# Performance work log

Hardware: AMD Instinct MI355X
Metric: run time of the kernel (lower is better)

## Reference

```python
import jax, jax.numpy as jnp
import numpy as np

B, T, D, K = 4, 2048, 1024, 64


def _spectral_filters(seq_len, k):
    # Hankel matrix Z_ij = 2 / ((i+j)^3 - (i+j)), top-k eig-pairs scaled by sigma^0.25
    e = np.arange(1, seq_len + 1, dtype=np.float64)
    ipj = e[:, None] + e[None, :]
    Z = 2.0 / (ipj ** 3 - ipj)
    sig, phi = np.linalg.eigh(Z)
    sig_k = np.clip(sig[-k:], 1e-9, None)
    return (phi[:, -k:] * sig_k ** 0.25).astype(np.float32)


def setup_inputs() -> dict:
    key = jax.random.key(0)
    ks = jax.random.split(key, 6)
    filt = jnp.asarray(_spectral_filters(T, K))  # [T, K]
    inp = {
        "x": jax.random.normal(ks[0], (B, T, D), dtype=jnp.float32),
        "W_pre": jax.random.normal(ks[1], (D, T), dtype=jnp.float32) / np.sqrt(D),
        "b_pre": jnp.zeros((T,), dtype=jnp.float32),
        "Q_filt": filt,
        "K_filt": jnp.array(filt),
        "W_v": jax.random.normal(ks[2], (D, K), dtype=jnp.float32) / np.sqrt(D),
        "b_v": jnp.zeros((K,), dtype=jnp.float32),
        "W_o": jax.random.normal(ks[3], (K, D), dtype=jnp.float32) / np.sqrt(K),
        "b_o": jnp.zeros((D,), dtype=jnp.float32),
        "decay": jnp.ones((T,), dtype=jnp.float32),
    }
    return inp


def reference(x, W_pre, b_pre, Q_filt, K_filt, W_v, b_v, W_o, b_o, decay):
    # pre-projection d_model -> seq_len (since d_model != seq_len)
    x_proj = x @ W_pre + b_pre                      # [B, T, T]
    Q = jnp.einsum('bti,ik->btk', x_proj, Q_filt)   # [B, T, K]
    Kf = jnp.einsum('bti,ik->btk', x_proj, K_filt)  # [B, T, K]
    V = x @ W_v + b_v                               # [B, T, K]
    # outer-product state with per-timestep decay, prefix-summed over time
    Z = jnp.einsum('btp,btn->btpn', V, Kf) * decay[None, :, None, None]  # [B,T,K,K]
    H = jnp.cumsum(Z, axis=1)                       # [B, T, K, K]
    Y = jnp.einsum('btk,btkn->btn', Q, H)           # [B, T, K]
    return Y @ W_o + b_o                            # [B, T, D]
```

## Files before the change

kernel.cpp:

```cpp
#include <hip/hip_runtime.h>

#define TS 2048
#define DM 1024
#define KD 64
#define NB 4

#define WTH_OFF 0
#define WTL_OFF 98304
#define BC_OFF  196608
#define QKV_OFF 196864
#define P_OFF   1769728
#define PF_OFF  (P_OFF)
#define O_OFF   (P_OFF)
#define ST_OFF  (P_OFF + 1048576)
#define YB_OFF  (P_OFF + 2097152)

typedef __attribute__((ext_vector_type(8))) short bf16x8;
typedef __attribute__((ext_vector_type(4))) float f32x4;

__device__ __forceinline__ ushort f2bf(float f) {
  unsigned u = __float_as_uint(f);
  unsigned r = u + 0x7FFFu + ((u >> 16) & 1u);
  return (ushort)(r >> 16);
}
__device__ __forceinline__ float bf2f(ushort h) {
  return __uint_as_float(((unsigned)h) << 16);
}

__global__ __launch_bounds__(256) void k_prep(
    const float* __restrict__ W_pre, const float* __restrict__ Qf,
    const float* __restrict__ Kf, float* __restrict__ Pf) {
  const int d0 = blockIdx.x * 64;
  const int f = blockIdx.y;
  const int ks = blockIdx.z;
  const float* __restrict__ F = f ? Kf : Qf;
  const int tid = threadIdx.x;
  const int wave = tid >> 6, lane = tid & 63;
  const int quad = lane >> 4, l15 = lane & 15;
  __shared__ ushort As[64 * 72];
  __shared__ ushort Bs[64 * 72];
  f32x4 acc[4];
#pragma unroll
  for (int nt = 0; nt < 4; ++nt) acc[nt] = (f32x4){0.f, 0.f, 0.f, 0.f};

  const int ra = tid >> 3;
  const int c4 = (tid & 7) * 4;
  float4 aw[2];
  float bw[8];
  int t0 = ks * 128;
#pragma unroll
  for (int i = 0; i < 2; ++i)
    aw[i] = *(const float4*)&W_pre[(size_t)(d0 + i * 32 + ra) * TS + t0 + c4];
#pragma unroll
  for (int h = 0; h < 2; ++h)
#pragma unroll
    for (int u = 0; u < 4; ++u)
      bw[h * 4 + u] = F[(size_t)(t0 + (wave + 4 * h) * 4 + u) * KD + lane];

  for (int step = 0; step < 4; ++step) {
    __syncthreads();
#pragma unroll
    for (int i = 0; i < 2; ++i) {
      const int r = i * 32 + ra;
      const float4 v = aw[i];
      const ushort h0 = f2bf(v.x), h1 = f2bf(v.y), h2 = f2bf(v.z), h3 = f2bf(v.w);
      *(ushort4*)&As[r * 72 + c4] = make_ushort4(h0, h1, h2, h3);
      *(ushort4*)&As[r * 72 + 32 + c4] = make_ushort4(
          f2bf(v.x - bf2f(h0)), f2bf(v.y - bf2f(h1)),
          f2bf(v.z - bf2f(h2)), f2bf(v.w - bf2f(h3)));
    }
#pragma unroll
    for (int h = 0; h < 2; ++h) {
      const int gg = wave + 4 * h;
      ushort hh[4], ll[4];
#pragma unroll
      for (int u = 0; u < 4; ++u) {
        hh[u] = f2bf(bw[h * 4 + u]);
        ll[u] = f2bf(bw[h * 4 + u] - bf2f(hh[u]));
      }
      *(ushort4*)&Bs[lane * 72 + gg * 4] = make_ushort4(hh[0], hh[1], hh[2], hh[3]);
      *(ushort4*)&Bs[lane * 72 + 32 + gg * 4] = make_ushort4(ll[0], ll[1], ll[2], ll[3]);
    }
    __syncthreads();
    if (step < 3) {
      const int t1 = t0 + 32;
#pragma unroll
      for (int i = 0; i < 2; ++i)
        aw[i] = *(const float4*)&W_pre[(size_t)(d0 + i * 32 + ra) * TS + t1 + c4];
#pragma unroll
      for (int h = 0; h < 2; ++h)
#pragma unroll
        for (int u = 0; u < 4; ++u)
          bw[h * 4 + u] = F[(size_t)(t1 + (wave + 4 * h) * 4 + u) * KD + lane];
    }
    const ushort* ap = &As[(wave * 16 + l15) * 72 + quad * 8];
    const bf16x8 a_h = *(const bf16x8*)ap;
    const bf16x8 a_l = *(const bf16x8*)(ap + 32);
#pragma unroll
    for (int nt = 0; nt < 4; ++nt) {
      const ushort* bp = &Bs[(nt * 16 + l15) * 72 + quad * 8];
      const bf16x8 b_h = *(const bf16x8*)bp;
      const bf16x8 b_l = *(const bf16x8*)(bp + 32);
      acc[nt] = __builtin_amdgcn_mfma_f32_16x16x32_bf16(a_h, b_h, acc[nt], 0, 0, 0);
      acc[nt] = __builtin_amdgcn_mfma_f32_16x16x32_bf16(a_h, b_l, acc[nt], 0, 0, 0);
      acc[nt] = __builtin_amdgcn_mfma_f32_16x16x32_bf16(a_l, b_h, acc[nt], 0, 0, 0);
    }
    t0 += 32;
  }
#pragma unroll
  for (int nt = 0; nt < 4; ++nt) {
    const int n = f * 64 + nt * 16 + l15;
#pragma unroll
    for (int r = 0; r < 4; ++r) {
      const int d = d0 + wave * 16 + quad * 4 + r;
      Pf[((size_t)ks * 128 + n) * DM + d] = acc[nt][r];
    }
  }
}

__global__ __launch_bounds__(256) void k_fred(
    const float* __restrict__ Pf, const float* __restrict__ Wv,
    const float* __restrict__ b_pre, const float* __restrict__ Qf,
    const float* __restrict__ Kf, const float* __restrict__ bv,
    ushort* __restrict__ WT_hi, ushort* __restrict__ WT_lo,
    float* __restrict__ bcomb) {
  const int bx = blockIdx.x;
  const int tid = threadIdx.x;
  if (bx < 32) {
    const int n0 = bx * 4;
    const int d4 = tid * 4;
#pragma unroll
    for (int j = 0; j < 4; ++j) {
      const int n = n0 + j;
      float4 s = {0.f, 0.f, 0.f, 0.f};
#pragma unroll
      for (int ks = 0; ks < 16; ++ks) {
        const float4 v = *(const float4*)&Pf[((size_t)ks * 128 + n) * DM + d4];
        s.x += v.x; s.y += v.y; s.z += v.z; s.w += v.w;
      }
      const ushort h0 = f2bf(s.x), h1 = f2bf(s.y), h2 = f2bf(s.z), h3 = f2bf(s.w);
      *(ushort4*)&WT_hi[(size_t)n * DM + d4] = make_ushort4(h0, h1, h2, h3);
      *(ushort4*)&WT_lo[(size_t)n * DM + d4] = make_ushort4(
          f2bf(s.x - bf2f(h0)), f2bf(s.y - bf2f(h1)),
          f2bf(s.z - bf2f(h2)), f2bf(s.w - bf2f(h3)));
    }
    const float* __restrict__ F = (n0 < 64) ? Qf : Kf;
    const int c0 = n0 & 63;
    __shared__ float bred[4][256];
    float p[4] = {0.f, 0.f, 0.f, 0.f};
#pragma unroll
    for (int u = 0; u < 8; ++u) {
      const int t = tid * 8 + u;
      const float bp = b_pre[t];
#pragma unroll
      for (int j = 0; j < 4; ++j) p[j] += bp * F[(size_t)t * KD + c0 + j];
    }
#pragma unroll
    for (int j = 0; j < 4; ++j) bred[j][tid] = p[j];
    __syncthreads();
    for (int s = 128; s > 0; s >>= 1) {
      if (tid < s) {
#pragma unroll
        for (int j = 0; j < 4; ++j) bred[j][tid] += bred[j][tid + s];
      }
      __syncthreads();
    }
    if (tid < 4) bcomb[n0 + tid] = bred[tid][0];
  } else {
    const int n0 = 128 + (bx - 32) * 4;
    const int d4 = tid * 4;
#pragma unroll
    for (int j = 0; j < 4; ++j) {
      const int c = n0 - 128 + j;
      float v[4];
#pragma unroll
      for (int i = 0; i < 4; ++i) v[i] = Wv[(size_t)(d4 + i) * KD + c];
      const ushort h0 = f2bf(v[0]), h1 = f2bf(v[1]), h2 = f2bf(v[2]), h3 = f2bf(v[3]);
      *(ushort4*)&WT_hi[(size_t)(n0 + j) * DM + d4] = make_ushort4(h0, h1, h2, h3);
      *(ushort4*)&WT_lo[(size_t)(n0 + j) * DM + d4] = make_ushort4(
          f2bf(v[0] - bf2f(h0)), f2bf(v[1] - bf2f(h1)),
          f2bf(v[2] - bf2f(h2)), f2bf(v[3] - bf2f(h3)));
    }
    if (tid < 4) bcomb[n0 + tid] = bv[n0 - 128 + tid];
  }
}

__global__ __launch_bounds__(256) void k_qkv(
    const float* __restrict__ x, const ushort* __restrict__ WT_hi,
    const ushort* __restrict__ WT_lo, float* __restrict__ P) {
  const int row0 = blockIdx.x * 64;
  const int ks = blockIdx.y;
  const int tid = threadIdx.x;
  const int wave = tid >> 6, lane = tid & 63;
  const int quad = lane >> 4, l15 = lane & 15;
  const int n0 = wave * 48;
  __shared__ ushort As[64 * 72];
  __shared__ ushort Bs[192 * 72];
  f32x4 acc[4][3];
#pragma unroll
  for (int mt = 0; mt < 4; ++mt)
#pragma unroll
    for (int nt = 0; nt < 3; ++nt) acc[mt][nt] = (f32x4){0.f, 0.f, 0.f, 0.f};

  for (int step = 0; step < 8; ++step) {
    const int kk = ks * 256 + step * 32;
    __syncthreads();
#pragma unroll
    for (int i = 0; i < 2; ++i) {
      const int idx = i * 256 + tid;
      const int r = idx >> 3, c4 = (idx & 7) * 4;
      const float4 v = *(const float4*)&x[(size_t)(row0 + r) * DM + kk + c4];
      const ushort h0 = f2bf(v.x), h1 = f2bf(v.y), h2 = f2bf(v.z), h3 = f2bf(v.w);
      *(ushort4*)&As[r * 72 + c4] = make_ushort4(h0, h1, h2, h3);
      *(ushort4*)&As[r * 72 + 32 + c4] = make_ushort4(
          f2bf(v.x - bf2f(h0)), f2bf(v.y - bf2f(h1)),
          f2bf(v.z - bf2f(h2)), f2bf(v.w - bf2f(h3)));
    }
#pragma unroll
    for (int i = 0; i < 6; ++i) {
      const int idx = i * 256 + tid;
      const int half = idx >= 768;
      const int j = half ? idx - 768 : idx;
      const int n = j >> 2, ch = j & 3;
      const ushort* src = (half ? WT_lo : WT_hi) + (size_t)n * DM + kk + ch * 8;
      *(float4*)&Bs[n * 72 + half * 32 + ch * 8] = *(const float4*)src;
    }
    __syncthreads();
    bf16x8 a_h[4], a_l[4], b_h[3], b_l[3];
#pragma unroll
    for (int mt = 0; mt < 4; ++mt) {
      const ushort* p = &As[(mt * 16 + l15) * 72 + quad * 8];
      a_h[mt] = *(const bf16x8*)p;
      a_l[mt] = *(const bf16x8*)(p + 32);
    }
#pragma unroll
    for (int nt = 0; nt < 3; ++nt) {
      const ushort* p = &Bs[(n0 + nt * 16 + l15) * 72 + quad * 8];
      b_h[nt] = *(const bf16x8*)p;
      b_l[nt] = *(const bf16x8*)(p + 32);
    }
#pragma unroll
    for (int mt = 0; mt < 4; ++mt)
#pragma unroll
      for (int nt = 0; nt < 3; ++nt) {
        acc[mt][nt] = __builtin_amdgcn_mfma_f32_16x16x32_bf16(a_h[mt], b_h[nt], acc[mt][nt], 0, 0, 0);
        acc[mt][nt] = __builtin_amdgcn_mfma_f32_16x16x32_bf16(a_h[mt], b_l[nt], acc[mt][nt], 0, 0, 0);
        acc[mt][nt] = __builtin_amdgcn_mfma_f32_16x16x32_bf16(a_l[mt], b_h[nt], acc[mt][nt], 0, 0, 0);
      }
  }
  float* Pp = P + (size_t)ks * TS * NB * 192;
#pragma unroll
  for (int mt = 0; mt < 4; ++mt) {
    const int rbase = row0 + mt * 16 + quad * 4;
#pragma unroll
    for (int nt = 0; nt < 3; ++nt) {
      const int col = n0 + nt * 16 + l15;
#pragma unroll
      for (int r = 0; r < 4; ++r)
        Pp[(size_t)(rbase + r) * 192 + col] = acc[mt][nt][r];
    }
  }
}

__global__ __launch_bounds__(256) void k_red(const float* __restrict__ P,
                                             const float* __restrict__ bcomb,
                                             float* __restrict__ QKV) {
  const int f4 = blockIdx.x * 256 + threadIdx.x;
  const int g = f4 * 4;
  const int col = g % 192;
  const size_t NTOT = (size_t)TS * NB * 192;
  float4 a = *(const float4*)&P[g];
  const float4 b = *(const float4*)&P[NTOT + g];
  const float4 c = *(const float4*)&P[2 * NTOT + g];
  const float4 d = *(const float4*)&P[3 * NTOT + g];
  const float4 bi = *(const float4*)&bcomb[col];
  a.x += b.x + c.x + d.x + bi.x;
  a.y += b.y + c.y + d.y + bi.y;
  a.z += b.z + c.z + d.z + bi.z;
  a.w += b.w + c.w + d.w + bi.w;
  *(float4*)&QKV[g] = a;
}

__global__ __launch_bounds__(256) void k_chunk(
    const float* __restrict__ QKV, const float* __restrict__ decay,
    float* __restrict__ Yb, float* __restrict__ O) {
  const int c = blockIdx.x;
  const int b = blockIdx.y;
  const int s0 = c * 32;
  const int tid = threadIdx.x;
  __shared__ float Qs[32][68], Ks[32][68], Vs[32][68];
  __shared__ float Ss[32][36];
  __shared__ float dec[32];

  for (int idx = tid; idx < 32 * 16; idx += 256) {
    const int r = idx >> 4, q = (idx & 15) * 4;
    const size_t base = (size_t)(b * TS + s0 + r) * 192;
    *(float4*)&Qs[r][q] = *(const float4*)&QKV[base + q];
    *(float4*)&Ks[r][q] = *(const float4*)&QKV[base + 64 + q];
    *(float4*)&Vs[r][q] = *(const float4*)&QKV[base + 128 + q];
  }
  if (tid < 32) dec[tid] = decay[s0 + tid];
  __syncthreads();

  {
    const int sc = (tid & 15) * 2;
    const int tr = (tid >> 4) * 2;
    float a00 = 0.f, a01 = 0.f, a10 = 0.f, a11 = 0.f;
#pragma unroll
    for (int k = 0; k < 64; k += 4) {
      const float4 q0 = *(const float4*)&Qs[tr][k];
      const float4 q1 = *(const float4*)&Qs[tr + 1][k];
      const float4 v0 = *(const float4*)&Vs[sc][k];
      const float4 v1 = *(const float4*)&Vs[sc + 1][k];
      a00 += q0.x * v0.x + q0.y * v0.y + q0.z * v0.z + q0.w * v0.w;
      a01 += q0.x * v1.x + q0.y * v1.y + q0.z * v1.z + q0.w * v1.w;
      a10 += q1.x * v0.x + q1.y * v0.y + q1.z * v0.z + q1.w * v0.w;
      a11 += q1.x * v1.x + q1.y * v1.y + q1.z * v1.z + q1.w * v1.w;
    }
    const float d0 = dec[sc], d1 = dec[sc + 1];
    Ss[tr][sc]         = (sc     <= tr)     ? a00 * d0 : 0.f;
    Ss[tr][sc + 1]     = (sc + 1 <= tr)     ? a01 * d1 : 0.f;
    Ss[tr + 1][sc]     = (sc     <= tr + 1) ? a10 * d0 : 0.f;
    Ss[tr + 1][sc + 1] = (sc + 1 <= tr + 1) ? a11 * d1 : 0.f;
  }

  float o[4][4];
#pragma unroll
  for (int i = 0; i < 4; ++i)
#pragma unroll
    for (int j = 0; j < 4; ++j) o[i][j] = 0.f;
  {
    const int kx = (tid & 15) * 4;
    const int nx = (tid >> 4) * 4;
#pragma unroll
    for (int s = 0; s < 32; ++s) {
      const float ds = dec[s];
      float4 v4 = *(const float4*)&Vs[s][kx];
      const float4 k4 = *(const float4*)&Ks[s][nx];
      v4.x *= ds; v4.y *= ds; v4.z *= ds; v4.w *= ds;
      o[0][0] += v4.x * k4.x; o[0][1] += v4.x * k4.y; o[0][2] += v4.x * k4.z; o[0][3] += v4.x * k4.w;
      o[1][0] += v4.y * k4.x; o[1][1] += v4.y * k4.y; o[1][2] += v4.y * k4.z; o[1][3] += v4.y * k4.w;
      o[2][0] += v4.z * k4.x; o[2][1] += v4.z * k4.y; o[2][2] += v4.z * k4.z; o[2][3] += v4.z * k4.w;
      o[3][0] += v4.w * k4.x; o[3][1] += v4.w * k4.y; o[3][2] += v4.w * k4.z; o[3][3] += v4.w * k4.w;
    }
  }
  __syncthreads();

  {
    const int nx = (tid & 15) * 4;
    const int tr = (tid >> 4) * 2;
    float y0[4] = {0.f, 0.f, 0.f, 0.f};
    float y1[4] = {0.f, 0.f, 0.f, 0.f};
#pragma unroll
    for (int s = 0; s < 32; s += 4) {
      const float4 sa = *(const float4*)&Ss[tr][s];
      const float4 sb = *(const float4*)&Ss[tr + 1][s];
#pragma unroll
      for (int u = 0; u < 4; ++u) {
        const float4 k4 = *(const float4*)&Ks[s + u][nx];
        const float su0 = (u == 0) ? sa.x : (u == 1) ? sa.y : (u == 2) ? sa.z : sa.w;
        const float su1 = (u == 0) ? sb.x : (u == 1) ? sb.y : (u == 2) ? sb.z : sb.w;
        y0[0] += su0 * k4.x; y0[1] += su0 * k4.y; y0[2] += su0 * k4.z; y0[3] += su0 * k4.w;
        y1[0] += su1 * k4.x; y1[1] += su1 * k4.y; y1[2] += su1 * k4.z; y1[3] += su1 * k4.w;
      }
    }
    float4 w0, w1;
    w0.x = y0[0]; w0.y = y0[1]; w0.z = y0[2]; w0.w = y0[3];
    w1.x = y1[0]; w1.y = y1[1]; w1.z = y1[2]; w1.w = y1[3];
    *(float4*)&Yb[(size_t)(b * TS + s0 + tr) * KD + nx] = w0;
    *(float4*)&Yb[(size_t)(b * TS + s0 + tr + 1) * KD + nx] = w1;
  }

  {
    const int kx = (tid & 15) * 4;
    const int nx = (tid >> 4) * 4;
    const size_t base = ((size_t)(b * 64 + c) * 64) * 64;
#pragma unroll
    for (int i = 0; i < 4; ++i) {
      float4 w;
      w.x = o[i][0]; w.y = o[i][1]; w.z = o[i][2]; w.w = o[i][3];
      *(float4*)&O[base + (size_t)(kx + i) * 64 + nx] = w;
    }
  }
}

__global__ __launch_bounds__(256) void k_scan(const float* __restrict__ O,
                                              float* __restrict__ State) {
  const int e = blockIdx.x * 256 + threadIdx.x;
  const int b = blockIdx.y;
  const float* op = O + (size_t)b * 64 * 4096 + e;
  float* sp = State + (size_t)b * 64 * 4096 + e;
  float run = 0.f;
  for (int c = 0; c < 64; ++c) {
    sp[(size_t)c * 4096] = run;
    run += op[(size_t)c * 4096];
  }
}

__global__ __launch_bounds__(256) void k_inter(const float* __restrict__ QKV,
                                               const float* __restrict__ State,
                                               float* __restrict__ Yb) {
  const int tt = blockIdx.x;
  const int b = blockIdx.y;
  const int t0 = tt * 32;
  const int tid = threadIdx.x;
  __shared__ float Sts[64][68];
  __shared__ float Qs[32][68];
  for (int idx = tid; idx < 1024; idx += 256) {
    const int k = idx >> 4, n = (idx & 15) * 4;
    *(float4*)&Sts[k][n] =
        *(const float4*)&State[(size_t)(b * 64 + tt) * 4096 + (size_t)k * 64 + n];
  }
  for (int idx = tid; idx < 512; idx += 256) {
    const int r = idx >> 4, q = (idx & 15) * 4;
    *(float4*)&Qs[r][q] = *(const float4*)&QKV[(size_t)(b * TS + t0 + r) * 192 + q];
  }
  __syncthreads();
  const int nx = (tid & 15) * 4;
  const int tr = (tid >> 4) * 2;
  float y0[4] = {0.f, 0.f, 0.f, 0.f};
  float y1[4] = {0.f, 0.f, 0.f, 0.f};
#pragma unroll
  for (int k = 0; k < 64; k += 4) {
    const float4 q0 = *(const float4*)&Qs[tr][k];
    const float4 q1 = *(const float4*)&Qs[tr + 1][k];
#pragma unroll
    for (int u = 0; u < 4; ++u) {
      const float4 st = *(const float4*)&Sts[k + u][nx];
      const float a0 = (u == 0) ? q0.x : (u == 1) ? q0.y : (u == 2) ? q0.z : q0.w;
      const float a1 = (u == 0) ? q1.x : (u == 1) ? q1.y : (u == 2) ? q1.z : q1.w;
      y0[0] += a0 * st.x; y0[1] += a0 * st.y; y0[2] += a0 * st.z; y0[3] += a0 * st.w;
      y1[0] += a1 * st.x; y1[1] += a1 * st.y; y1[2] += a1 * st.z; y1[3] += a1 * st.w;
    }
  }
  float4 p0 = *(const float4*)&Yb[(size_t)(b * TS + t0 + tr) * KD + nx];
  float4 p1 = *(const float4*)&Yb[(size_t)(b * TS + t0 + tr + 1) * KD + nx];
  p0.x += y0[0]; p0.y += y0[1]; p0.z += y0[2]; p0.w += y0[3];
  p1.x += y1[0]; p1.y += y1[1]; p1.z += y1[2]; p1.w += y1[3];
  *(float4*)&Yb[(size_t)(b * TS + t0 + tr) * KD + nx] = p0;
  *(float4*)&Yb[(size_t)(b * TS + t0 + tr + 1) * KD + nx] = p1;
}

__global__ __launch_bounds__(256) void k_out(const float* __restrict__ Yb,
                                             const float* __restrict__ Wo,
                                             const float* __restrict__ bo,
                                             float* __restrict__ out) {
  const int row0 = blockIdx.x * 16;
  const int tid = threadIdx.x;
  __shared__ float Ys[16][68];
  {
    const int r = tid >> 4, q = (tid & 15) * 4;
    *(float4*)&Ys[r][q] = *(const float4*)&Yb[(size_t)(row0 + r) * KD + q];
  }
  __syncthreads();
  const int d0 = tid * 4;
  float acc[16][4];
#pragma unroll
  for (int r = 0; r < 16; ++r)
#pragma unroll
    for (int j = 0; j < 4; ++j) acc[r][j] = 0.f;
  for (int k = 0; k < 64; k += 4) {
    const float4 w0 = *(const float4*)&Wo[(size_t)(k + 0) * DM + d0];
    const float4 w1 = *(const float4*)&Wo[(size_t)(k + 1) * DM + d0];
    const float4 w2 = *(const float4*)&Wo[(size_t)(k + 2) * DM + d0];
    const float4 w3 = *(const float4*)&Wo[(size_t)(k + 3) * DM + d0];
#pragma unroll
    for (int r = 0; r < 16; ++r) {
      const float4 ys = *(const float4*)&Ys[r][k];
      acc[r][0] += ys.x * w0.x + ys.y * w1.x + ys.z * w2.x + ys.w * w3.x;
      acc[r][1] += ys.x * w0.y + ys.y * w1.y + ys.z * w2.y + ys.w * w3.y;
      acc[r][2] += ys.x * w0.z + ys.y * w1.z + ys.z * w2.z + ys.w * w3.z;
      acc[r][3] += ys.x * w0.w + ys.y * w1.w + ys.z * w2.w + ys.w * w3.w;
    }
  }
  const float4 b4 = *(const float4*)&bo[d0];
#pragma unroll
  for (int r = 0; r < 16; ++r) {
    float4 w;
    w.x = acc[r][0] + b4.x;
    w.y = acc[r][1] + b4.y;
    w.z = acc[r][2] + b4.z;
    w.w = acc[r][3] + b4.w;
    *(float4*)&out[(size_t)(row0 + r) * DM + d0] = w;
  }
}

extern "C" void kernel_launch(void* const* d_in, const int* in_sizes, int n_in,
                              void* d_out, int out_size, void* d_ws, size_t ws_size,
                              hipStream_t stream) {
  const float* x     = (const float*)d_in[0];
  const float* W_pre = (const float*)d_in[1];
  const float* b_pre = (const float*)d_in[2];
  const float* Qf    = (const float*)d_in[3];
  const float* Kf    = (const float*)d_in[4];
  const float* W_v   = (const float*)d_in[5];
  const float* b_v   = (const float*)d_in[6];
  const float* W_o   = (const float*)d_in[7];
  const float* b_o   = (const float*)d_in[8];
  const float* decay = (const float*)d_in[9];
  float* out = (float*)d_out;
  float* ws = (float*)d_ws;

  ushort* WT_hi = (ushort*)(ws + WTH_OFF);
  ushort* WT_lo = (ushort*)(ws + WTL_OFF);
  float* bcomb = ws + BC_OFF;
  float* QKV   = ws + QKV_OFF;
  float* P     = ws + P_OFF;
  float* Pf    = ws + PF_OFF;
  float* O     = ws + O_OFF;
  float* St    = ws + ST_OFF;
  float* Yb    = ws + YB_OFF;

  k_prep<<<dim3(16, 2, 16), 256, 0, stream>>>(W_pre, Qf, Kf, Pf);
  k_fred<<<dim3(48), 256, 0, stream>>>(Pf, W_v, b_pre, Qf, Kf, b_v,
                                       WT_hi, WT_lo, bcomb);
  k_qkv<<<dim3(NB * TS / 64, 4), 256, 0, stream>>>(x, WT_hi, WT_lo, P);
  k_red<<<dim3(NB * TS * 192 / 4 / 256), 256, 0, stream>>>(P, bcomb, QKV);
  k_chunk<<<dim3(TS / 32, NB), 256, 0, stream>>>(QKV, decay, Yb, O);
  k_scan<<<dim3(16, NB), 256, 0, stream>>>(O, St);
  k_inter<<<dim3(TS / 32, NB), 256, 0, stream>>>(QKV, St, Yb);
  k_out<<<dim3(NB * TS / 16), 256, 0, stream>>>(Yb, W_o, b_o, out);
}
```

Baseline: 186.6 us.

## Fuse split-K reduction into chunk kernel and merge scan, inter, output projection

Folds the split-K partial-sum reduction into the chunk kernel, so Q/K/V go straight into shared memory and only Q is written back. The separate scan, inter-chunk and output-projection kernels become one kernel: each block sums all preceding chunk states itself, applies the state to its queries, and does the W_o projection from shared memory. This removes three launches and several global round trips (QKV, State, Yb rewrite). The cost is redundant prefix summation of up to 63 chunk states per block, which is quadratic work with load imbalance across chunks, and larger shared-memory use per block.

```diff
diff --git a/kernel.cpp b/kernel.cpp
--- a/kernel.cpp
+++ b/kernel.cpp
@@ -8,12 +8,11 @@
 #define WTH_OFF 0
 #define WTL_OFF 98304
 #define BC_OFF  196608
-#define QKV_OFF 196864
+#define QG_OFF  196864
 #define P_OFF   1769728
 #define PF_OFF  (P_OFF)
-#define O_OFF   (P_OFF)
-#define ST_OFF  (P_OFF + 1048576)
-#define YB_OFF  (P_OFF + 2097152)
+#define O_OFF   8061184
+#define YB_OFF  9109760
 
 typedef __attribute__((ext_vector_type(8))) short bf16x8;
 typedef __attribute__((ext_vector_type(4))) float f32x4;
@@ -262,27 +261,9 @@
   }
 }
 
-__global__ __launch_bounds__(256) void k_red(const float* __restrict__ P,
-                                             const float* __restrict__ bcomb,
-                                             float* __restrict__ QKV) {
-  const int f4 = blockIdx.x * 256 + threadIdx.x;
-  const int g = f4 * 4;
-  const int col = g % 192;
-  const size_t NTOT = (size_t)TS * NB * 192;
-  float4 a = *(const float4*)&P[g];
-  const float4 b = *(const float4*)&P[NTOT + g];
-  const float4 c = *(const float4*)&P[2 * NTOT + g];
-  const float4 d = *(const float4*)&P[3 * NTOT + g];
-  const float4 bi = *(const float4*)&bcomb[col];
-  a.x += b.x + c.x + d.x + bi.x;
-  a.y += b.y + c.y + d.y + bi.y;
-  a.z += b.z + c.z + d.z + bi.z;
-  a.w += b.w + c.w + d.w + bi.w;
-  *(float4*)&QKV[g] = a;
-}
-
-__global__ __launch_bounds__(256) void k_chunk(
-    const float* __restrict__ QKV, const float* __restrict__ decay,
+__global__ __launch_bounds__(256) void k_chunkred(
+    const float* __restrict__ P, const float* __restrict__ bcomb,
+    const float* __restrict__ decay, float* __restrict__ Qg,
     float* __restrict__ Yb, float* __restrict__ O) {
   const int c = blockIdx.x;
   const int b = blockIdx.y;
@@ -291,13 +272,28 @@
   __shared__ float Qs[32][68], Ks[32][68], Vs[32][68];
   __shared__ float Ss[32][36];
   __shared__ float dec[32];
-
-  for (int idx = tid; idx < 32 * 16; idx += 256) {
-    const int r = idx >> 4, q = (idx & 15) * 4;
-    const size_t base = (size_t)(b * TS + s0 + r) * 192;
-    *(float4*)&Qs[r][q] = *(const float4*)&QKV[base + q];
-    *(float4*)&Ks[r][q] = *(const float4*)&QKV[base + 64 + q];
-    *(float4*)&Vs[r][q] = *(const float4*)&QKV[base + 128 + q];
+  const size_t NTOT = (size_t)TS * NB * 192;
+
+  for (int idx = tid; idx < 32 * 48; idx += 256) {
+    const int r = idx / 48, cq = (idx % 48) * 4;
+    const size_t g = (size_t)(b * TS + s0 + r) * 192 + cq;
+    float4 a = *(const float4*)&P[g];
+    const float4 b2 = *(const float4*)&P[NTOT + g];
+    const float4 c2 = *(const float4*)&P[2 * NTOT + g];
+    const float4 d2 = *(const float4*)&P[3 * NTOT + g];
+    const float4 bi = *(const float4*)&bcomb[cq];
+    a.x += b2.x + c2.x + d2.x + bi.x;
+    a.y += b2.y + c2.y + d2.y + bi.y;
+    a.z += b2.z + c2.z + d2.z + bi.z;
+    a.w += b2.w + c2.w + d2.w + bi.w;
+    if (cq < 64) {
+      *(float4*)&Qs[r][cq] = a;
+      *(float4*)&Qg[(size_t)(b * TS + s0 + r) * KD + cq] = a;
+    } else if (cq < 128) {
+      *(float4*)&Ks[r][cq - 64] = a;
+    } else {
+      *(float4*)&Vs[r][cq - 128] = a;
+    }
   }
   if (tid < 32) dec[tid] = decay[s0 + tid];
   __syncthreads();
@@ -384,104 +380,101 @@
   }
 }
 
-__global__ __launch_bounds__(256) void k_scan(const float* __restrict__ O,
-                                              float* __restrict__ State) {
-  const int e = blockIdx.x * 256 + threadIdx.x;
+__global__ __launch_bounds__(256) void k_interout(
+    const float* __restrict__ O, const float* __restrict__ Qg,
+    const float* __restrict__ Yb, const float* __restrict__ Wo,
+    const float* __restrict__ bo, float* __restrict__ out) {
+  const int c = blockIdx.x;
   const int b = blockIdx.y;
-  const float* op = O + (size_t)b * 64 * 4096 + e;
-  float* sp = State + (size_t)b * 64 * 4096 + e;
-  float run = 0.f;
-  for (int c = 0; c < 64; ++c) {
-    sp[(size_t)c * 4096] = run;
-    run += op[(size_t)c * 4096];
-  }
-}
-
-__global__ __launch_bounds__(256) void k_inter(const float* __restrict__ QKV,
-                                               const float* __restrict__ State,
-                                               float* __restrict__ Yb) {
-  const int tt = blockIdx.x;
-  const int b = blockIdx.y;
-  const int t0 = tt * 32;
+  const int t0 = c * 32;
   const int tid = threadIdx.x;
   __shared__ float Sts[64][68];
   __shared__ float Qs[32][68];
-  for (int idx = tid; idx < 1024; idx += 256) {
-    const int k = idx >> 4, n = (idx & 15) * 4;
-    *(float4*)&Sts[k][n] =
-        *(const float4*)&State[(size_t)(b * 64 + tt) * 4096 + (size_t)k * 64 + n];
-  }
-  for (int idx = tid; idx < 512; idx += 256) {
+  __shared__ float Yrow[32][68];
+
+  float4 st[4];
+#pragma unroll
+  for (int g = 0; g < 4; ++g) st[g] = (float4){0.f, 0.f, 0.f, 0.f};
+  const size_t ob = (size_t)b * 64 * 4096;
+  for (int cp = 0; cp < c; ++cp) {
+#pragma unroll
+    for (int g = 0; g < 4; ++g) {
+      const float4 v = *(const float4*)&O[ob + (size_t)cp * 4096 + g * 1024 + tid * 4];
+      st[g].x += v.x; st[g].y += v.y; st[g].z += v.z; st[g].w += v.w;
+    }
+  }
+#pragma unroll
+  for (int g = 0; g < 4; ++g)
+    *(float4*)&Sts[g * 16 + (tid >> 4)][(tid & 15) * 4] = st[g];
+
+#pragma unroll
+  for (int i = 0; i < 2; ++i) {
+    const int idx = i * 256 + tid;
     const int r = idx >> 4, q = (idx & 15) * 4;
-    *(float4*)&Qs[r][q] = *(const float4*)&QKV[(size_t)(b * TS + t0 + r) * 192 + q];
+    *(float4*)&Qs[r][q] = *(const float4*)&Qg[(size_t)(b * TS + t0 + r) * KD + q];
+    *(float4*)&Yrow[r][q] = *(const float4*)&Yb[(size_t)(b * TS + t0 + r) * KD + q];
   }
   __syncthreads();
-  const int nx = (tid & 15) * 4;
-  const int tr = (tid >> 4) * 2;
-  float y0[4] = {0.f, 0.f, 0.f, 0.f};
-  float y1[4] = {0.f, 0.f, 0.f, 0.f};
-#pragma unroll
-  for (int k = 0; k < 64; k += 4) {
-    const float4 q0 = *(const float4*)&Qs[tr][k];
-    const float4 q1 = *(const float4*)&Qs[tr + 1][k];
-#pragma unroll
-    for (int u = 0; u < 4; ++u) {
-      const float4 st = *(const float4*)&Sts[k + u][nx];
-      const float a0 = (u == 0) ? q0.x : (u == 1) ? q0.y : (u == 2) ? q0.z : q0.w;
-      const float a1 = (u == 0) ? q1.x : (u == 1) ? q1.y : (u == 2) ? q1.z : q1.w;
-      y0[0] += a0 * st.x; y0[1] += a0 * st.y; y0[2] += a0 * st.z; y0[3] += a0 * st.w;
-      y1[0] += a1 * st.x; y1[1] += a1 * st.y; y1[2] += a1 * st.z; y1[3] += a1 * st.w;
-    }
-  }
-  float4 p0 = *(const float4*)&Yb[(size_t)(b * TS + t0 + tr) * KD + nx];
-  float4 p1 = *(const float4*)&Yb[(size_t)(b * TS + t0 + tr + 1) * KD + nx];
-  p0.x += y0[0]; p0.y += y0[1]; p0.z += y0[2]; p0.w += y0[3];
-  p1.x += y1[0]; p1.y += y1[1]; p1.z += y1[2]; p1.w += y1[3];
-  *(float4*)&Yb[(size_t)(b * TS + t0 + tr) * KD + nx] = p0;
-  *(float4*)&Yb[(size_t)(b * TS + t0 + tr + 1) * KD + nx] = p1;
-}
-
-__global__ __launch_bounds__(256) void k_out(const float* __restrict__ Yb,
-                                             const float* __restrict__ Wo,
-                                             const float* __restrict__ bo,
-                                             float* __restrict__ out) {
-  const int row0 = blockIdx.x * 16;
-  const int tid = threadIdx.x;
-  __shared__ float Ys[16][68];
+
   {
-    const int r = tid >> 4, q = (tid & 15) * 4;
-    *(float4*)&Ys[r][q] = *(const float4*)&Yb[(size_t)(row0 + r) * KD + q];
+    const int nx = (tid & 15) * 4;
+    const int tr = (tid >> 4) * 2;
+    float y0[4] = {0.f, 0.f, 0.f, 0.f};
+    float y1[4] = {0.f, 0.f, 0.f, 0.f};
+#pragma unroll
+    for (int k = 0; k < 64; k += 4) {
+      const float4 q0 = *(const float4*)&Qs[tr][k];
+      const float4 q1 = *(const float4*)&Qs[tr + 1][k];
+#pragma unroll
+      for (int u = 0; u < 4; ++u) {
+        const float4 s4 = *(const float4*)&Sts[k + u][nx];
+        const float a0 = (u == 0) ? q0.x : (u == 1) ? q0.y : (u == 2) ? q0.z : q0.w;
+        const float a1 = (u == 0) ? q1.x : (u == 1) ? q1.y : (u == 2) ? q1.z : q1.w;
+        y0[0] += a0 * s4.x; y0[1] += a0 * s4.y; y0[2] += a0 * s4.z; y0[3] += a0 * s4.w;
+        y1[0] += a1 * s4.x; y1[1] += a1 * s4.y; y1[2] += a1 * s4.z; y1[3] += a1 * s4.w;
+      }
+    }
+    float4 p0 = *(const float4*)&Yrow[tr][nx];
+    float4 p1 = *(const float4*)&Yrow[tr + 1][nx];
+    p0.x += y0[0]; p0.y += y0[1]; p0.z += y0[2]; p0.w += y0[3];
+    p1.x += y1[0]; p1.y += y1[1]; p1.z += y1[2]; p1.w += y1[3];
+    *(float4*)&Yrow[tr][nx] = p0;
+    *(float4*)&Yrow[tr + 1][nx] = p1;
   }
   __syncthreads();
+
   const int d0 = tid * 4;
-  float acc[16][4];
-#pragma unroll
-  for (int r = 0; r < 16; ++r)
-#pragma unroll
-    for (int j = 0; j < 4; ++j) acc[r][j] = 0.f;
-  for (int k = 0; k < 64; k += 4) {
-    const float4 w0 = *(const float4*)&Wo[(size_t)(k + 0) * DM + d0];
-    const float4 w1 = *(const float4*)&Wo[(size_t)(k + 1) * DM + d0];
-    const float4 w2 = *(const float4*)&Wo[(size_t)(k + 2) * DM + d0];
-    const float4 w3 = *(const float4*)&Wo[(size_t)(k + 3) * DM + d0];
+  const float4 b4 = *(const float4*)&bo[d0];
+#pragma unroll
+  for (int pass = 0; pass < 2; ++pass) {
+    float acc[16][4];
+#pragma unroll
+    for (int r = 0; r < 16; ++r)
+#pragma unroll
+      for (int j = 0; j < 4; ++j) acc[r][j] = 0.f;
+    for (int k = 0; k < 64; k += 4) {
+      const float4 w0 = *(const float4*)&Wo[(size_t)(k + 0) * DM + d0];
+      const float4 w1 = *(const float4*)&Wo[(size_t)(k + 1) * DM + d0];
+      const float4 w2 = *(const float4*)&Wo[(size_t)(k + 2) * DM + d0];
+      const float4 w3 = *(const float4*)&Wo[(size_t)(k + 3) * DM + d0];
+#pragma unroll
+      for (int r = 0; r < 16; ++r) {
+        const float4 ys = *(const float4*)&Yrow[pass * 16 + r][k];
+        acc[r][0] += ys.x * w0.x + ys.y * w1.x + ys.z * w2.x + ys.w * w3.x;
+        acc[r][1] += ys.x * w0.y + ys.y * w1.y + ys.z * w2.y + ys.w * w3.y;
+        acc[r][2] += ys.x * w0.z + ys.y * w1.z + ys.z * w2.z + ys.w * w3.z;
+        acc[r][3] += ys.x * w0.w + ys.y * w1.w + ys.z * w2.w + ys.w * w3.w;
+      }
+    }
 #pragma unroll
     for (int r = 0; r < 16; ++r) {
-      const float4 ys = *(const float4*)&Ys[r][k];
-      acc[r][0] += ys.x * w0.x + ys.y * w1.x + ys.z * w2.x + ys.w * w3.x;
-      acc[r][1] += ys.x * w0.y + ys.y * w1.y + ys.z * w2.y + ys.w * w3.y;
-      acc[r][2] += ys.x * w0.z + ys.y * w1.z + ys.z * w2.z + ys.w * w3.z;
-      acc[r][3] += ys.x * w0.w + ys.y * w1.w + ys.z * w2.w + ys.w * w3.w;
-    }
-  }
-  const float4 b4 = *(const float4*)&bo[d0];
-#pragma unroll
-  for (int r = 0; r < 16; ++r) {
-    float4 w;
-    w.x = acc[r][0] + b4.x;
-    w.y = acc[r][1] + b4.y;
-    w.z = acc[r][2] + b4.z;
-    w.w = acc[r][3] + b4.w;
-    *(float4*)&out[(size_t)(row0 + r) * DM + d0] = w;
+      float4 w;
+      w.x = acc[r][0] + b4.x;
+      w.y = acc[r][1] + b4.y;
+      w.z = acc[r][2] + b4.z;
+      w.w = acc[r][3] + b4.w;
+      *(float4*)&out[(size_t)(b * TS + t0 + pass * 16 + r) * DM + d0] = w;
+    }
   }
 }
 
@@ -504,20 +497,16 @@
   ushort* WT_hi = (ushort*)(ws + WTH_OFF);
   ushort* WT_lo = (ushort*)(ws + WTL_OFF);
   float* bcomb = ws + BC_OFF;
-  float* QKV   = ws + QKV_OFF;
+  float* Qg    = ws + QG_OFF;
   float* P     = ws + P_OFF;
   float* Pf    = ws + PF_OFF;
   float* O     = ws + O_OFF;
-  float* St    = ws + ST_OFF;
   float* Yb    = ws + YB_OFF;
 
   k_prep<<<dim3(16, 2, 16), 256, 0, stream>>>(W_pre, Qf, Kf, Pf);
   k_fred<<<dim3(48), 256, 0, stream>>>(Pf, W_v, b_pre, Qf, Kf, b_v,
                                        WT_hi, WT_lo, bcomb);
   k_qkv<<<dim3(NB * TS / 64, 4), 256, 0, stream>>>(x, WT_hi, WT_lo, P);
-  k_red<<<dim3(NB * TS * 192 / 4 / 256), 256, 0, stream>>>(P, bcomb, QKV);
-  k_chunk<<<dim3(TS / 32, NB), 256, 0, stream>>>(QKV, decay, Yb, O);
-  k_scan<<<dim3(16, NB), 256, 0, stream>>>(O, St);
-  k_inter<<<dim3(TS / 32, NB), 256, 0, stream>>>(QKV, St, Yb);
-  k_out<<<dim3(NB * TS / 16), 256, 0, stream>>>(Yb, W_o, b_o, out);
-}
+  k_chunkred<<<dim3(TS / 32, NB), 256, 0, stream>>>(P, bcomb, decay, Qg, Yb, O);
+  k_interout<<<dim3(TS / 32, NB), 256, 0, stream>>>(O, Qg, Yb, W_o, b_o, out);
+}
```

Measured after the change: 204.9 us. 1.1x slower.
